# Kernel tuning notes

Hardware: AMD Instinct MI355X
Metric: run time of the kernel (lower is better)

## Reference

```python
import jax, jax.numpy as jnp
import numpy as np

HIDDEN = 1024
HEADS = 16
HEAD_DIM = HIDDEN // HEADS
SCALE = float(np.sqrt(HEAD_DIM))


def setup_inputs() -> dict:
    key = jax.random.key(0)
    ks = jax.random.split(key, 9)
    B, S = 4, 8192
    std = 1.0 / np.sqrt(HIDDEN)
    x = jax.random.normal(ks[0], (B, S, HIDDEN), dtype=jnp.float32)
    Wq = jax.random.normal(ks[1], (HIDDEN, HIDDEN), dtype=jnp.float32) * std
    Wk = jax.random.normal(ks[2], (HIDDEN, HIDDEN), dtype=jnp.float32) * std
    Wv = jax.random.normal(ks[3], (HIDDEN, HIDDEN), dtype=jnp.float32) * std
    Wo = jax.random.normal(ks[4], (HIDDEN, HIDDEN), dtype=jnp.float32) * std
    bq = jax.random.normal(ks[5], (HIDDEN,), dtype=jnp.float32) * std
    bk = jax.random.normal(ks[6], (HIDDEN,), dtype=jnp.float32) * std
    bv = jax.random.normal(ks[7], (HIDDEN,), dtype=jnp.float32) * std
    bo = jax.random.normal(ks[8], (HIDDEN,), dtype=jnp.float32) * std
    return {"x": x, "Wq": Wq, "bq": bq, "Wk": Wk, "bk": bk,
            "Wv": Wv, "bv": bv, "Wo": Wo, "bo": bo}


def reference(x, Wq, bq, Wk, bk, Wv, bv, Wo, bo):
    B, S, E = x.shape
    H, D = HEADS, HEAD_DIM
    # torch nn.Linear: y = x @ W^T + b
    q = (jnp.einsum('bse,fe->bsf', x, Wq) + bq).reshape(B, S, H, D)
    k = (jnp.einsum('bse,fe->bsf', x, Wk) + bk).reshape(B, S, H, D)
    v = (jnp.einsum('bse,fe->bsf', x, Wv) + bv).reshape(B, S, H, D)
    # Faithful to source: NO head transpose, so matmul contracts over head_dim
    # with (B,S) as batch dims -> per-token head-mixing scores [B,S,H,H].
    scores = jnp.einsum('bshd,bsgd->bshg', q, k) / SCALE
    probs = jax.nn.softmax(scores, axis=-1)
    attn = jnp.einsum('bshg,bsgd->bshd', probs, v).reshape(B, S, E)
    return jnp.einsum('bse,fe->bsf', attn, Wo) + bo
```

## Files before the change

### kernel.cpp

```cpp
#include <hip/hip_runtime.h>
#include <hip/hip_bf16.h>
#include <cstdint>
#include <type_traits>

#define GLOBAL_AS __attribute__((address_space(1)))
#define LDS_AS    __attribute__((address_space(3)))

typedef short bf16x8 __attribute__((ext_vector_type(8)));
typedef short short8_t __attribute__((ext_vector_type(8)));
typedef float f32x4  __attribute__((ext_vector_type(4)));

static constexpr int E_DIM = 1024;
static constexpr int HD = 64;
static constexpr int QKV_STRIDE = 3072;
static constexpr int KDIM = 1024;
static constexpr int NTK  = KDIM / 64;
static constexpr int NIT  = NTK / 2;

__device__ __forceinline__ float b2f(short s) {
    union { unsigned u; float f; } x;
    x.u = ((unsigned)(unsigned short)s) << 16;
    return x.f;
}
__device__ __forceinline__ short f2b(float f) {
    union { float f; unsigned u; } x; x.f = f;
    unsigned r = x.u + 0x7FFF + ((x.u >> 16) & 1);
    return (short)(r >> 16);
}

__global__ __launch_bounds__(256) void k_prep(
    const float* __restrict__ x,
    const float* __restrict__ Wq, const float* __restrict__ Wk,
    const float* __restrict__ Wv, const float* __restrict__ Wo,
    const float* __restrict__ bq, const float* __restrict__ bk,
    const float* __restrict__ bv,
    short* __restrict__ xb, short* __restrict__ Wqkvb, short* __restrict__ Wob,
    float* __restrict__ bqkv, int n4x, int n4w)
{
    int i = blockIdx.x * 256 + threadIdx.x;
    const float* src;
    short* dst;
    int j;
    if (i < n4x)                       { src = x;  dst = xb;                  j = i; }
    else if (i < n4x + n4w)            { src = Wq; dst = Wqkvb;               j = i - n4x; }
    else if (i < n4x + 2 * n4w)        { src = Wk; dst = Wqkvb + 4 * n4w;     j = i - n4x - n4w; }
    else if (i < n4x + 3 * n4w)        { src = Wv; dst = Wqkvb + 8 * n4w;     j = i - n4x - 2 * n4w; }
    else if (i < n4x + 4 * n4w)        { src = Wo; dst = Wob;                 j = i - n4x - 3 * n4w; }
    else {
        int b = i - (n4x + 4 * n4w);
        if (b < 768) {
            #pragma unroll
            for (int e = 0; e < 4; ++e) {
                int idx = b * 4 + e;
                float v = (idx < 1024) ? bq[idx] : (idx < 2048 ? bk[idx - 1024] : bv[idx - 2048]);
                bqkv[idx] = v;
            }
        }
        return;
    }
    float4 v = reinterpret_cast<const float4*>(src)[j];
    short4 o;
    o.x = f2b(v.x); o.y = f2b(v.y); o.z = f2b(v.z); o.w = f2b(v.w);
    reinterpret_cast<short4*>(dst)[j] = o;
}

template <typename OutT>
__global__ __launch_bounds__(512, 2) void k_gemm256(
    const short* __restrict__ A,
    const short* __restrict__ Bm,
    const float* __restrict__ bias,
    OutT* __restrict__ C,
    int NT_N, int N)
{
    __shared__ short lds[65536];

    const int tid  = threadIdx.x;
    const int lane = tid & 63;
    const int wv   = tid >> 6;
    const int wr   = wv >> 2;
    const int wc   = wv & 3;
    const int frow = lane & 15;
    const int ks   = lane >> 4;
    const int sw   = frow & 7;
    const int sl0  = ((0 + ks) ^ sw) * 8;
    const int sl1  = ((4 + ks) ^ sw) * 8;

    const int nwg = gridDim.x, nper = nwg >> 3, bid = blockIdx.x;
    const int swz = (bid & 7) * nper + (bid >> 3);
    const int m0  = (swz / NT_N) * 256;
    const int n0  = (swz % NT_N) * 256;

    const int ArdBase = wr * 8192;
    const int BrdBase = 16384 + (wc >> 1) * 8192 + (wc & 1) * 4096;

    const int srow = tid >> 3;
    const int ssl  = ((tid & 7) ^ (srow & 7)) * 8;
    const int sdst = tid * 8;

#define GLD(SRC, DST) __builtin_amdgcn_global_load_lds(                            \
        (const GLOBAL_AS short*)(SRC), (LDS_AS short*)(DST), 16, 0, 0)
#define STAGE_A(BUF, HALF, T) do {                                                 \
    const short* s_ = A + (size_t)(m0 + (HALF) * 128 + srow) * KDIM + (T) * 64 + ssl; \
    short* d_ = &lds[(BUF) * 32768 + (HALF) * 8192 + sdst];                        \
    GLD(s_, d_);  GLD(s_ + (size_t)64 * KDIM, d_ + 4096);                          \
} while (0)
#define STAGE_B(BUF, HALF, T) do {                                                 \
    const short* s_ = Bm + (size_t)(n0 + (HALF) * 128 + srow) * KDIM + (T) * 64 + ssl; \
    short* d_ = &lds[(BUF) * 32768 + 16384 + (HALF) * 8192 + sdst];                \
    GLD(s_, d_);  GLD(s_ + (size_t)64 * KDIM, d_ + 4096);                          \
} while (0)

#define RD_A(BUF, MIB) do {                                                        \
    _Pragma("unroll")                                                              \
    for (int m_ = 0; m_ < 4; ++m_) {                                               \
        const short* p_ = &lds[(BUF) * 32768 + ArdBase + ((MIB) + m_) * 1024 + frow * 64]; \
        af[m_][0] = *(const bf16x8*)(p_ + sl0);                                    \
        af[m_][1] = *(const bf16x8*)(p_ + sl1);                                    \
    }                                                                              \
} while (0)
#define RD_B(BUF, NIB, BF) do {                                                    \
    _Pragma("unroll")                                                              \
    for (int n_ = 0; n_ < 2; ++n_) {                                               \
        const short* p_ = &lds[(BUF) * 32768 + BrdBase + ((NIB) + n_) * 1024 + frow * 64]; \
        BF[n_][0] = *(const bf16x8*)(p_ + sl0);                                    \
        BF[n_][1] = *(const bf16x8*)(p_ + sl1);                                    \
    }                                                                              \
} while (0)

#define MM(MB, NB, BF) do {                                                        \
    __builtin_amdgcn_s_setprio(1);                                                 \
    _Pragma("unroll")                                                              \
    for (int m_ = 0; m_ < 4; ++m_)                                                 \
        _Pragma("unroll")                                                          \
        for (int n_ = 0; n_ < 2; ++n_) {                                           \
            acc[(MB)+m_][(NB)+n_] = __builtin_amdgcn_mfma_f32_16x16x32_bf16(       \
                af[m_][0], BF[n_][0], acc[(MB)+m_][(NB)+n_], 0, 0, 0);             \
            acc[(MB)+m_][(NB)+n_] = __builtin_amdgcn_mfma_f32_16x16x32_bf16(       \
                af[m_][1], BF[n_][1], acc[(MB)+m_][(NB)+n_], 0, 0, 0);             \
        }                                                                          \
    __builtin_amdgcn_s_setprio(0);                                                 \
} while (0)

#define BAR   __builtin_amdgcn_s_barrier()
#define VM4   asm volatile("s_waitcnt vmcnt(4)" ::: "memory")
#define VM6   asm volatile("s_waitcnt vmcnt(6)" ::: "memory")

    f32x4 acc[8][4];
    #pragma unroll
    for (int i = 0; i < 8; ++i)
        #pragma unroll
        for (int j = 0; j < 4; ++j)
            acc[i][j] = (f32x4){0.f, 0.f, 0.f, 0.f};

    bf16x8 af[4][2], bfA[2][2], bfB[2][2];

    STAGE_B(0, 0, 0);  STAGE_B(0, 1, 0);
    STAGE_A(0, 0, 0);  STAGE_A(0, 1, 0);
    STAGE_B(1, 0, 1);  STAGE_B(1, 1, 1);
    STAGE_A(1, 0, 1);
    VM6;  BAR;
    RD_A(0, 0);  RD_B(0, 0, bfA);

    #pragma unroll 1
    for (int it = 0; it < NIT; ++it) {
        const int ta = 2 * it + 1;
        const int tb = (2 * it + 2 <= 15) ? 2 * it + 2 : 15;
        const int tc = (2 * it + 3 <= 15) ? 2 * it + 3 : 15;

        BAR;
        MM(0, 0, bfA);
        RD_B(0, 2, bfB);
        STAGE_A(1, 1, ta);
        BAR;
        MM(0, 2, bfB);
        RD_A(0, 4);
        STAGE_B(0, 0, tb);
        BAR;
        MM(4, 0, bfA);
        STAGE_B(0, 1, tb);
        VM4;
        BAR;
        MM(4, 2, bfB);
        RD_A(1, 0);  RD_B(1, 0, bfA);
        STAGE_A(0, 0, tb);
        BAR;
        MM(0, 0, bfA);
        RD_B(1, 2, bfB);
        STAGE_A(0, 1, tb);
        BAR;
        MM(0, 2, bfB);
        RD_A(1, 4);
        STAGE_B(1, 0, tc);
        BAR;
        MM(4, 0, bfA);
        STAGE_B(1, 1, tc);
        VM4;
        BAR;
        MM(4, 2, bfB);
        RD_A(0, 0);  RD_B(0, 0, bfA);
        STAGE_A(1, 0, tc);
    }

    asm volatile("s_waitcnt vmcnt(0)" ::: "memory");

    const int crow = (lane >> 4) * 4;
    const int ccol = lane & 15;
    float bv4[4];
    #pragma unroll
    for (int ni = 0; ni < 4; ++ni)
        bv4[ni] = bias[n0 + wc * 64 + ni * 16 + ccol];
    #pragma unroll
    for (int mi = 0; mi < 8; ++mi) {
        #pragma unroll
        for (int r = 0; r < 4; ++r) {
            const size_t rowg = (size_t)(m0 + wr * 128 + mi * 16 + crow + r) * N;
            #pragma unroll
            for (int ni = 0; ni < 4; ++ni) {
                const int col = n0 + wc * 64 + ni * 16 + ccol;
                float v = acc[mi][ni][r] + bv4[ni];
                if constexpr (std::is_same<OutT, float>::value) {
                    C[rowg + col] = v;
                } else {
                    C[rowg + col] = f2b(v);
                }
            }
        }
    }
#undef GLD
#undef STAGE_A
#undef STAGE_B
#undef RD_A
#undef RD_B
#undef MM
#undef BAR
#undef VM4
#undef VM6
}

__global__ __launch_bounds__(256) void k_attn(
    const short* __restrict__ QKV, short* __restrict__ O)
{
    __shared__ short Ks[16][1032];
    __shared__ short Vs[16][1032];

    const int tid = threadIdx.x;
    const int tok0 = blockIdx.x * 16;

    for (int i = tid; i < 2048; i += 256) {
        int t = i >> 7;
        int j = i & 127;
        const size_t base = (size_t)(tok0 + t) * QKV_STRIDE;
        *reinterpret_cast<short8_t*>(&Ks[t][j * 8]) =
            *reinterpret_cast<const short8_t*>(&QKV[base + 1024 + j * 8]);
        *reinterpret_cast<short8_t*>(&Vs[t][j * 8]) =
            *reinterpret_cast<const short8_t*>(&QKV[base + 2048 + j * 8]);
    }
    __syncthreads();

    const int tl = tid >> 4;
    const int h  = tid & 15;

    float qf[64];
    const short* qp = QKV + (size_t)(tok0 + tl) * QKV_STRIDE + h * HD;
    #pragma unroll
    for (int i = 0; i < 8; ++i) {
        short8_t v = *reinterpret_cast<const short8_t*>(&qp[i * 8]);
        #pragma unroll
        for (int j = 0; j < 8; ++j) qf[i * 8 + j] = b2f(v[j]);
    }

    float s[16];
    #pragma unroll
    for (int g = 0; g < 16; ++g) {
        float a = 0.f;
        #pragma unroll
        for (int i = 0; i < 8; ++i) {
            short8_t kv = *reinterpret_cast<const short8_t*>(&Ks[tl][g * HD + i * 8]);
            #pragma unroll
            for (int j = 0; j < 8; ++j) a += qf[i * 8 + j] * b2f(kv[j]);
        }
        s[g] = a * 0.125f;
    }
    float mx = s[0];
    #pragma unroll
    for (int g = 1; g < 16; ++g) mx = fmaxf(mx, s[g]);
    float l = 0.f;
    #pragma unroll
    for (int g = 0; g < 16; ++g) { s[g] = __expf(s[g] - mx); l += s[g]; }
    const float inv = 1.f / l;
    #pragma unroll
    for (int g = 0; g < 16; ++g) s[g] *= inv;

    short* op = O + (size_t)(tok0 + tl) * E_DIM + h * HD;
    #pragma unroll
    for (int c = 0; c < 4; ++c) {
        float a[16];
        #pragma unroll
        for (int j = 0; j < 16; ++j) a[j] = 0.f;
        #pragma unroll
        for (int g = 0; g < 16; ++g) {
            short8_t v0 = *reinterpret_cast<const short8_t*>(&Vs[tl][g * HD + c * 16]);
            short8_t v1 = *reinterpret_cast<const short8_t*>(&Vs[tl][g * HD + c * 16 + 8]);
            #pragma unroll
            for (int j = 0; j < 8; ++j) {
                a[j]     += s[g] * b2f(v0[j]);
                a[8 + j] += s[g] * b2f(v1[j]);
            }
        }
        short8_t o0, o1;
        #pragma unroll
        for (int j = 0; j < 8; ++j) { o0[j] = f2b(a[j]); o1[j] = f2b(a[8 + j]); }
        *reinterpret_cast<short8_t*>(&op[c * 16])     = o0;
        *reinterpret_cast<short8_t*>(&op[c * 16 + 8]) = o1;
    }
}

extern "C" void kernel_launch(void* const* d_in, const int* in_sizes, int n_in,
                              void* d_out, int out_size, void* d_ws, size_t ws_size,
                              hipStream_t stream) {
    const float* x  = (const float*)d_in[0];
    const float* Wq = (const float*)d_in[1];
    const float* bq = (const float*)d_in[2];
    const float* Wk = (const float*)d_in[3];
    const float* bk = (const float*)d_in[4];
    const float* Wv = (const float*)d_in[5];
    const float* bv = (const float*)d_in[6];
    const float* Wo = (const float*)d_in[7];
    const float* bo = (const float*)d_in[8];
    float* out = (float*)d_out;

    const int T = in_sizes[0] / E_DIM;
    char* ws = (char*)d_ws;
    const size_t SZ_X    = (size_t)T * E_DIM * 2;
    const size_t SZ_WQKV = (size_t)3 * E_DIM * E_DIM * 2;
    const size_t SZ_W    = (size_t)E_DIM * E_DIM * 2;
    const size_t SZ_B    = 3072 * sizeof(float) + 4096;

    short* xb    = (short*)(ws);
    short* Wqkvb = (short*)(ws + SZ_X);
    short* Wob   = (short*)(ws + SZ_X + SZ_WQKV);
    float* bqkv  = (float*)(ws + SZ_X + SZ_WQKV + SZ_W);
    short* QKVb  = (short*)(ws + SZ_X + SZ_WQKV + SZ_W + SZ_B);
    short* Ab    = xb;

    const int n4x = T * E_DIM / 4;
    const int n4w = E_DIM * E_DIM / 4;
    const int nprep = n4x + 4 * n4w + 768;
    k_prep<<<dim3((nprep + 255) / 256), dim3(256), 0, stream>>>(
        x, Wq, Wk, Wv, Wo, bq, bk, bv, xb, Wqkvb, Wob, bqkv, n4x, n4w);

    k_gemm256<short><<<dim3((T / 256) * (QKV_STRIDE / 256)), dim3(512), 0, stream>>>(
        xb, Wqkvb, bqkv, QKVb, QKV_STRIDE / 256, QKV_STRIDE);

    k_attn<<<dim3(T / 16), dim3(256), 0, stream>>>(QKVb, Ab);

    k_gemm256<float><<<dim3((T / 256) * (E_DIM / 256)), dim3(512), 0, stream>>>(
        Ab, Wob, bo, out, E_DIM / 256, E_DIM);
}
```

Measured before the change: 387.7 us.

## Restructure GEMM main loop into four phases with fused MFMA blocks

Reschedules the bf16 GEMM main loop from eight barrier-separated phases per iteration to four. Each phase now issues a merged 4x4 MFMA block using both B fragment sets. Global-to-LDS staging for both halves of a tile is grouped together, and the prologue preloads both buffers fully, with the vmcnt wait raised to 8. The aim is to cut barrier count and give MFMAs longer uninterrupted runs. The cost is more live fragment registers and coarser overlap of loads with compute.

```diff
diff --git a/kernel.cpp b/kernel.cpp
--- a/kernel.cpp
+++ b/kernel.cpp
@@ -127,23 +127,28 @@
     }                                                                              \
 } while (0)
 
-#define MM(MB, NB, BF) do {                                                        \
+#define MM2(MB) do {                                                               \
     __builtin_amdgcn_s_setprio(1);                                                 \
     _Pragma("unroll")                                                              \
-    for (int m_ = 0; m_ < 4; ++m_)                                                 \
+    for (int m_ = 0; m_ < 4; ++m_) {                                               \
         _Pragma("unroll")                                                          \
         for (int n_ = 0; n_ < 2; ++n_) {                                           \
-            acc[(MB)+m_][(NB)+n_] = __builtin_amdgcn_mfma_f32_16x16x32_bf16(       \
-                af[m_][0], BF[n_][0], acc[(MB)+m_][(NB)+n_], 0, 0, 0);             \
-            acc[(MB)+m_][(NB)+n_] = __builtin_amdgcn_mfma_f32_16x16x32_bf16(       \
-                af[m_][1], BF[n_][1], acc[(MB)+m_][(NB)+n_], 0, 0, 0);             \
+            acc[(MB)+m_][n_] = __builtin_amdgcn_mfma_f32_16x16x32_bf16(            \
+                af[m_][0], bfA[n_][0], acc[(MB)+m_][n_], 0, 0, 0);                 \
+            acc[(MB)+m_][n_] = __builtin_amdgcn_mfma_f32_16x16x32_bf16(            \
+                af[m_][1], bfA[n_][1], acc[(MB)+m_][n_], 0, 0, 0);                 \
+            acc[(MB)+m_][2+n_] = __builtin_amdgcn_mfma_f32_16x16x32_bf16(          \
+                af[m_][0], bfB[n_][0], acc[(MB)+m_][2+n_], 0, 0, 0);               \
+            acc[(MB)+m_][2+n_] = __builtin_amdgcn_mfma_f32_16x16x32_bf16(          \
+                af[m_][1], bfB[n_][1], acc[(MB)+m_][2+n_], 0, 0, 0);               \
         }                                                                          \
+    }                                                                              \
     __builtin_amdgcn_s_setprio(0);                                                 \
 } while (0)
 
 #define BAR   __builtin_amdgcn_s_barrier()
 #define VM4   asm volatile("s_waitcnt vmcnt(4)" ::: "memory")
-#define VM6   asm volatile("s_waitcnt vmcnt(6)" ::: "memory")
+#define VM8   asm volatile("s_waitcnt vmcnt(8)" ::: "memory")
 
     f32x4 acc[8][4];
     #pragma unroll
@@ -154,51 +159,34 @@
 
     bf16x8 af[4][2], bfA[2][2], bfB[2][2];
 
-    STAGE_B(0, 0, 0);  STAGE_B(0, 1, 0);
-    STAGE_A(0, 0, 0);  STAGE_A(0, 1, 0);
-    STAGE_B(1, 0, 1);  STAGE_B(1, 1, 1);
-    STAGE_A(1, 0, 1);
-    VM6;  BAR;
-    RD_A(0, 0);  RD_B(0, 0, bfA);
+    STAGE_A(0, 0, 0);  STAGE_A(0, 1, 0);  STAGE_B(0, 0, 0);  STAGE_B(0, 1, 0);
+    STAGE_A(1, 0, 1);  STAGE_A(1, 1, 1);  STAGE_B(1, 0, 1);  STAGE_B(1, 1, 1);
+    VM8;  BAR;
+    RD_A(0, 0);  RD_B(0, 0, bfA);  RD_B(0, 2, bfB);
 
     #pragma unroll 1
     for (int it = 0; it < NIT; ++it) {
-        const int ta = 2 * it + 1;
         const int tb = (2 * it + 2 <= 15) ? 2 * it + 2 : 15;
         const int tc = (2 * it + 3 <= 15) ? 2 * it + 3 : 15;
 
         BAR;
-        MM(0, 0, bfA);
-        RD_B(0, 2, bfB);
-        STAGE_A(1, 1, ta);
-        BAR;
-        MM(0, 2, bfB);
+        MM2(0);
         RD_A(0, 4);
-        STAGE_B(0, 0, tb);
-        BAR;
-        MM(4, 0, bfA);
-        STAGE_B(0, 1, tb);
+        STAGE_B(0, 0, tb);  STAGE_B(0, 1, tb);
         VM4;
         BAR;
-        MM(4, 2, bfB);
-        RD_A(1, 0);  RD_B(1, 0, bfA);
-        STAGE_A(0, 0, tb);
+        MM2(4);
+        STAGE_A(0, 0, tb);  STAGE_A(0, 1, tb);
+        RD_A(1, 0);  RD_B(1, 0, bfA);  RD_B(1, 2, bfB);
         BAR;
-        MM(0, 0, bfA);
-        RD_B(1, 2, bfB);
-        STAGE_A(0, 1, tb);
-        BAR;
-        MM(0, 2, bfB);
+        MM2(0);
         RD_A(1, 4);
-        STAGE_B(1, 0, tc);
-        BAR;
-        MM(4, 0, bfA);
-        STAGE_B(1, 1, tc);
+        STAGE_B(1, 0, tc);  STAGE_B(1, 1, tc);
         VM4;
         BAR;
-        MM(4, 2, bfB);
-        RD_A(0, 0);  RD_B(0, 0, bfA);
-        STAGE_A(1, 0, tc);
+        MM2(4);
+        STAGE_A(1, 0, tc);  STAGE_A(1, 1, tc);
+        RD_A(0, 0);  RD_B(0, 0, bfA);  RD_B(0, 2, bfB);
     }
 
     asm volatile("s_waitcnt vmcnt(0)" ::: "memory");
@@ -231,10 +219,10 @@
 #undef STAGE_B
 #undef RD_A
 #undef RD_B
-#undef MM
+#undef MM2
 #undef BAR
 #undef VM4
-#undef VM6
+#undef VM8
 }
 
 __global__ __launch_bounds__(256) void k_attn(
```

After: 393.5 us. Within noise of the previous version (+1.5%).

## Switch GEMM inner loop to 32x32x16 MFMA with re-planned LDS pipeline

Applied to the files above, without the earlier changes.

Replaces the 16x16x32 bf16 MFMA tiles in the 256x256 GEMM with 32x32x16 MFMA tiles, which changes the per-wave fragment layout, the LDS read pattern and the accumulator shape. The staging schedule is rebuilt around this, with different ordering of A/B prefetches and different vmcnt waits per phase. Larger MFMA tiles need fewer LDS fragment reads per FLOP and fewer instructions issued. The cost is a more complex epilogue mapping and possible LDS bank conflicts or pipeline hazards under the new schedule.

```diff
diff --git a/kernel.cpp b/kernel.cpp
--- a/kernel.cpp
+++ b/kernel.cpp
@@ -8,7 +8,7 @@
 
 typedef short bf16x8 __attribute__((ext_vector_type(8)));
 typedef short short8_t __attribute__((ext_vector_type(8)));
-typedef float f32x4  __attribute__((ext_vector_type(4)));
+typedef float f32x16 __attribute__((ext_vector_type(16)));
 
 static constexpr int E_DIM = 1024;
 static constexpr int HD = 64;
@@ -79,11 +79,9 @@
     const int wv   = tid >> 6;
     const int wr   = wv >> 2;
     const int wc   = wv & 3;
-    const int frow = lane & 15;
-    const int ks   = lane >> 4;
-    const int sw   = frow & 7;
-    const int sl0  = ((0 + ks) ^ sw) * 8;
-    const int sl1  = ((4 + ks) ^ sw) * 8;
+    const int arow = lane & 31;
+    const int kgrp = lane >> 5;
+    const int swz8 = arow & 7;
 
     const int nwg = gridDim.x, nper = nwg >> 3, bid = blockIdx.x;
     const int swz = (bid & 7) * nper + (bid >> 3);
@@ -110,56 +108,62 @@
     GLD(s_, d_);  GLD(s_ + (size_t)64 * KDIM, d_ + 4096);                          \
 } while (0)
 
-#define RD_A(BUF, MIB) do {                                                        \
+#define RD_A2(BUF, MB0, KH, DST) do {                                              \
     _Pragma("unroll")                                                              \
-    for (int m_ = 0; m_ < 4; ++m_) {                                               \
-        const short* p_ = &lds[(BUF) * 32768 + ArdBase + ((MIB) + m_) * 1024 + frow * 64]; \
-        af[m_][0] = *(const bf16x8*)(p_ + sl0);                                    \
-        af[m_][1] = *(const bf16x8*)(p_ + sl1);                                    \
+    for (int mb_ = 0; mb_ < 2; ++mb_) {                                            \
+        const int row_ = ((MB0) + mb_) * 32 + arow;                                \
+        const short* p_ = &lds[(BUF) * 32768 + ArdBase + row_ * 64];               \
+        _Pragma("unroll")                                                          \
+        for (int ks_ = 0; ks_ < 2; ++ks_)                                          \
+            DST[mb_][ks_] = *(const bf16x8*)(p_ +                                  \
+                ((((KH) * 4 + ks_ * 2 + kgrp) ^ swz8) * 8));                       \
     }                                                                              \
 } while (0)
-#define RD_B(BUF, NIB, BF) do {                                                    \
+#define RD_B2(BUF, KH, DST) do {                                                   \
     _Pragma("unroll")                                                              \
-    for (int n_ = 0; n_ < 2; ++n_) {                                               \
-        const short* p_ = &lds[(BUF) * 32768 + BrdBase + ((NIB) + n_) * 1024 + frow * 64]; \
-        BF[n_][0] = *(const bf16x8*)(p_ + sl0);                                    \
-        BF[n_][1] = *(const bf16x8*)(p_ + sl1);                                    \
+    for (int nb_ = 0; nb_ < 2; ++nb_) {                                            \
+        const int row_ = nb_ * 32 + arow;                                          \
+        const short* p_ = &lds[(BUF) * 32768 + BrdBase + row_ * 64];               \
+        _Pragma("unroll")                                                          \
+        for (int ks_ = 0; ks_ < 2; ++ks_)                                          \
+            DST[nb_][ks_] = *(const bf16x8*)(p_ +                                  \
+                ((((KH) * 4 + ks_ * 2 + kgrp) ^ swz8) * 8));                       \
     }                                                                              \
 } while (0)
 
-#define MM(MB, NB, BF) do {                                                        \
+#define MMQ(AF, BF, MH) do {                                                       \
     __builtin_amdgcn_s_setprio(1);                                                 \
     _Pragma("unroll")                                                              \
-    for (int m_ = 0; m_ < 4; ++m_)                                                 \
+    for (int mb_ = 0; mb_ < 2; ++mb_)                                              \
         _Pragma("unroll")                                                          \
-        for (int n_ = 0; n_ < 2; ++n_) {                                           \
-            acc[(MB)+m_][(NB)+n_] = __builtin_amdgcn_mfma_f32_16x16x32_bf16(       \
-                af[m_][0], BF[n_][0], acc[(MB)+m_][(NB)+n_], 0, 0, 0);             \
-            acc[(MB)+m_][(NB)+n_] = __builtin_amdgcn_mfma_f32_16x16x32_bf16(       \
-                af[m_][1], BF[n_][1], acc[(MB)+m_][(NB)+n_], 0, 0, 0);             \
+        for (int nb_ = 0; nb_ < 2; ++nb_) {                                        \
+            acc[(MH)*2+mb_][nb_] = __builtin_amdgcn_mfma_f32_32x32x16_bf16(        \
+                AF[mb_][0], BF[nb_][0], acc[(MH)*2+mb_][nb_], 0, 0, 0);            \
+            acc[(MH)*2+mb_][nb_] = __builtin_amdgcn_mfma_f32_32x32x16_bf16(        \
+                AF[mb_][1], BF[nb_][1], acc[(MH)*2+mb_][nb_], 0, 0, 0);            \
         }                                                                          \
     __builtin_amdgcn_s_setprio(0);                                                 \
 } while (0)
 
 #define BAR   __builtin_amdgcn_s_barrier()
+#define VM2   asm volatile("s_waitcnt vmcnt(2)" ::: "memory")
 #define VM4   asm volatile("s_waitcnt vmcnt(4)" ::: "memory")
-#define VM6   asm volatile("s_waitcnt vmcnt(6)" ::: "memory")
-
-    f32x4 acc[8][4];
-    #pragma unroll
-    for (int i = 0; i < 8; ++i)
-        #pragma unroll
-        for (int j = 0; j < 4; ++j)
-            acc[i][j] = (f32x4){0.f, 0.f, 0.f, 0.f};
-
-    bf16x8 af[4][2], bfA[2][2], bfB[2][2];
-
-    STAGE_B(0, 0, 0);  STAGE_B(0, 1, 0);
-    STAGE_A(0, 0, 0);  STAGE_A(0, 1, 0);
+
+    f32x16 acc[4][2];
+    #pragma unroll
+    for (int i = 0; i < 4; ++i)
+        #pragma unroll
+        for (int j = 0; j < 2; ++j)
+            #pragma unroll
+            for (int e = 0; e < 16; ++e)
+                acc[i][j][e] = 0.f;
+
+    bf16x8 afA[2][2], afB[2][2], bfA[2][2], bfB[2][2];
+
+    STAGE_A(0, 0, 0);  STAGE_A(0, 1, 0);  STAGE_B(0, 0, 0);  STAGE_B(0, 1, 0);
     STAGE_B(1, 0, 1);  STAGE_B(1, 1, 1);
-    STAGE_A(1, 0, 1);
-    VM6;  BAR;
-    RD_A(0, 0);  RD_B(0, 0, bfA);
+    VM4;  BAR;
+    RD_A2(0, 0, 0, afA);  RD_B2(0, 0, bfA);
 
     #pragma unroll 1
     for (int it = 0; it < NIT; ++it) {
@@ -168,60 +172,69 @@
         const int tc = (2 * it + 3 <= 15) ? 2 * it + 3 : 15;
 
         BAR;
-        MM(0, 0, bfA);
-        RD_B(0, 2, bfB);
+        MMQ(afA, bfA, 0);
+        RD_A2(0, 2, 0, afB);
+        STAGE_A(1, 0, ta);
+        BAR;
+        MMQ(afB, bfA, 1);
+        RD_A2(0, 0, 1, afA);
+        RD_B2(0, 1, bfB);
         STAGE_A(1, 1, ta);
         BAR;
-        MM(0, 2, bfB);
-        RD_A(0, 4);
+        MMQ(afA, bfB, 0);
+        RD_A2(0, 2, 1, afB);
         STAGE_B(0, 0, tb);
-        BAR;
-        MM(4, 0, bfA);
+        VM2;
+        BAR;
+        MMQ(afB, bfB, 1);
+        RD_A2(1, 0, 0, afA);
+        RD_B2(1, 0, bfA);
         STAGE_B(0, 1, tb);
-        VM4;
-        BAR;
-        MM(4, 2, bfB);
-        RD_A(1, 0);  RD_B(1, 0, bfA);
+        BAR;
+        MMQ(afA, bfA, 0);
+        RD_A2(1, 2, 0, afB);
         STAGE_A(0, 0, tb);
         BAR;
-        MM(0, 0, bfA);
-        RD_B(1, 2, bfB);
+        MMQ(afB, bfA, 1);
+        RD_A2(1, 0, 1, afA);
+        RD_B2(1, 1, bfB);
         STAGE_A(0, 1, tb);
         BAR;
-        MM(0, 2, bfB);
-        RD_A(1, 4);
+        MMQ(afA, bfB, 0);
+        RD_A2(1, 2, 1, afB);
         STAGE_B(1, 0, tc);
-        BAR;
-        MM(4, 0, bfA);
+        VM2;
+        BAR;
+        MMQ(afB, bfB, 1);
+        RD_A2(0, 0, 0, afA);
+        RD_B2(0, 0, bfA);
         STAGE_B(1, 1, tc);
-        VM4;
-        BAR;
-        MM(4, 2, bfB);
-        RD_A(0, 0);  RD_B(0, 0, bfA);
-        STAGE_A(1, 0, tc);
     }
 
     asm volatile("s_waitcnt vmcnt(0)" ::: "memory");
 
-    const int crow = (lane >> 4) * 4;
-    const int ccol = lane & 15;
-    float bv4[4];
-    #pragma unroll
-    for (int ni = 0; ni < 4; ++ni)
-        bv4[ni] = bias[n0 + wc * 64 + ni * 16 + ccol];
-    #pragma unroll
-    for (int mi = 0; mi < 8; ++mi) {
-        #pragma unroll
-        for (int r = 0; r < 4; ++r) {
-            const size_t rowg = (size_t)(m0 + wr * 128 + mi * 16 + crow + r) * N;
-            #pragma unroll
-            for (int ni = 0; ni < 4; ++ni) {
-                const int col = n0 + wc * 64 + ni * 16 + ccol;
-                float v = acc[mi][ni][r] + bv4[ni];
-                if constexpr (std::is_same<OutT, float>::value) {
-                    C[rowg + col] = v;
-                } else {
-                    C[rowg + col] = f2b(v);
+    float bv2[2];
+    #pragma unroll
+    for (int nb = 0; nb < 2; ++nb)
+        bv2[nb] = bias[n0 + wc * 64 + nb * 32 + arow];
+    #pragma unroll
+    for (int mb = 0; mb < 4; ++mb) {
+        #pragma unroll
+        for (int rg = 0; rg < 4; ++rg) {
+            #pragma unroll
+            for (int rr = 0; rr < 4; ++rr) {
+                const int r = rg * 4 + rr;
+                const size_t rowg =
+                    (size_t)(m0 + wr * 128 + mb * 32 + rr + rg * 8 + 4 * kgrp) * N;
+                #pragma unroll
+                for (int nb = 0; nb < 2; ++nb) {
+                    const int col = n0 + wc * 64 + nb * 32 + arow;
+                    float v = acc[mb][nb][r] + bv2[nb];
+                    if constexpr (std::is_same<OutT, float>::value) {
+                        C[rowg + col] = v;
+                    } else {
+                        C[rowg + col] = f2b(v);
+                    }
                 }
             }
         }
@@ -229,12 +242,12 @@
 #undef GLD
 #undef STAGE_A
 #undef STAGE_B
-#undef RD_A
-#undef RD_B
-#undef MM
+#undef RD_A2
+#undef RD_B2
+#undef MMQ
 #undef BAR
+#undef VM2
 #undef VM4
-#undef VM6
 }
 
 __global__ __launch_bounds__(256) void k_attn(
```

Result: slower. 413.1 us (+6.5%).
